# Kernel optimization log

Hardware: AMD Instinct MI355X
Metric: run time of the kernel (lower is better)

Reference implementation:

```python
import jax, jax.numpy as jnp
import numpy as np

B, H, S, D = 2, 16, 2048, 64


def setup_inputs() -> dict:
    key = jax.random.key(0)
    kq, kk, kv = jax.random.split(key, 3)
    q = jax.random.normal(kq, (B, H, S, D), dtype=jnp.float32)
    k = jax.random.normal(kk, (B, H, S, D), dtype=jnp.float32)
    v = jax.random.normal(kv, (B, H, S, D), dtype=jnp.float32)
    # look-ahead (causal) mask: 1 where attention is NOT allowed (future positions)
    mask = 1.0 - jnp.tril(jnp.ones((S, S), dtype=jnp.float32))
    mask = mask[None, None, :, :]  # broadcastable to (B, H, S, S)
    return {"q": q, "k": k, "v": v, "mask": mask}


def reference(q, k, v, mask):
    # scores: (B, H, Sq, Sk)
    dk = jnp.asarray(q.shape[-1], dtype=q.dtype)
    logits = jnp.einsum("bhqd,bhkd->bhqk", q, k) / jnp.sqrt(dk)
    logits = logits + mask * (-1e9)
    attn = jax.nn.softmax(logits, axis=-1)
    # dropout rate 0.0 / inference mode -> identity
    out = jnp.einsum("bhqk,bhkd->bhqd", attn, v)
    return out, attn
```

## Files before the change

### kernel.cpp

```cpp
#include <hip/hip_runtime.h>


typedef __attribute__((ext_vector_type(4))) float f32x4;
typedef __attribute__((ext_vector_type(8))) short bf16x8;

#define S_LEN 2048
#define D_DIM 64
#define LDK   72
#define SCALE 0.125f

__device__ __forceinline__ unsigned int f2bf1(float f) {
  unsigned int u = __float_as_uint(f);
  return (u + 0x7FFFu + ((u >> 16) & 1u)) >> 16;
}
__device__ __forceinline__ unsigned long long pack4bf(float a, float b, float c, float d) {
  unsigned int lo = f2bf1(a) | (f2bf1(b) << 16);
  unsigned int hi = f2bf1(c) | (f2bf1(d) << 16);
  return (unsigned long long)lo | ((unsigned long long)hi << 32);
}

__global__ __launch_bounds__(256, 4)
void attn_fused(const float* __restrict__ Qg, const float* __restrict__ Kg,
                const float* __restrict__ Vg, float* __restrict__ Og,
                float* __restrict__ Ag)
{
  __shared__ __attribute__((aligned(16))) unsigned short qs[64 * LDK];
  __shared__ __attribute__((aligned(16))) unsigned short ks[64 * LDK];
  __shared__ __attribute__((aligned(16))) unsigned short vs[64 * LDK];
  __shared__ __attribute__((aligned(16))) unsigned short ps[4 * 16 * LDK];

  const int tid  = threadIdx.x;
  const int lane = tid & 63;
  const int w    = tid >> 6;
  const int l15  = lane & 15;
  const int lg   = lane >> 4;
  const int bh   = blockIdx.x & 31;
  const int q0   = (blockIdx.x >> 5) << 6;

  const float* qb = Qg + (size_t)bh * S_LEN * D_DIM;
  const float* kb = Kg + (size_t)bh * S_LEN * D_DIM;
  const float* vb = Vg + (size_t)bh * S_LEN * D_DIM;
  float* ob = Og + (size_t)bh * S_LEN * D_DIM;
  float* ab = Ag + (size_t)bh * S_LEN * S_LEN;

#pragma unroll
  for (int j = 0; j < 4; ++j) {
    int f = tid + j * 256;
    int row = f >> 4, dg = f & 15;
    float4 v = *(const float4*)(qb + (q0 + row) * D_DIM + dg * 4);
    *(unsigned long long*)(qs + row * LDK + dg * 4) = pack4bf(v.x, v.y, v.z, v.w);
  }
  __syncthreads();
  const bf16x8 qf0 = *(const bf16x8*)(qs + (w * 16 + l15) * LDK + lg * 8);
  const bf16x8 qf1 = *(const bf16x8*)(qs + (w * 16 + l15) * LDK + 32 + lg * 8);

  const int ktiles = (q0 >> 6) + 1;
  const int qr0 = q0 + w * 16 + lg * 4;

  float lsum[4] = {0.f, 0.f, 0.f, 0.f};
  for (int t = 0; t < ktiles; ++t) {
    const int kt = t << 6;
    __syncthreads();
#pragma unroll
    for (int j = 0; j < 4; ++j) {
      int f = tid + j * 256;
      int row = f >> 4, dg = f & 15;
      float4 v = *(const float4*)(kb + (kt + row) * D_DIM + dg * 4);
      *(unsigned long long*)(ks + row * LDK + dg * 4) = pack4bf(v.x, v.y, v.z, v.w);
    }
    __syncthreads();
#pragma unroll
    for (int kbk = 0; kbk < 4; ++kbk) {
      const bf16x8 kf0 = *(const bf16x8*)(ks + (kbk * 16 + l15) * LDK + lg * 8);
      const bf16x8 kf1 = *(const bf16x8*)(ks + (kbk * 16 + l15) * LDK + 32 + lg * 8);
      f32x4 s = {0.f, 0.f, 0.f, 0.f};
      s = __builtin_amdgcn_mfma_f32_16x16x32_bf16(qf0, kf0, s, 0, 0, 0);
      s = __builtin_amdgcn_mfma_f32_16x16x32_bf16(qf1, kf1, s, 0, 0, 0);
      const int kc = kt + kbk * 16 + l15;
#pragma unroll
      for (int r = 0; r < 4; ++r)
        lsum[r] += (kc <= qr0 + r) ? __expf(s[r] * SCALE) : 0.f;
    }
  }
#pragma unroll
  for (int m = 1; m < 16; m <<= 1) {
#pragma unroll
    for (int r = 0; r < 4; ++r) lsum[r] += __shfl_xor(lsum[r], m, 64);
  }
  float ri[4];
#pragma unroll
  for (int r = 0; r < 4; ++r) ri[r] = 1.f / lsum[r];

  f32x4 o[4];
#pragma unroll
  for (int d = 0; d < 4; ++d) o[d] = (f32x4){0.f, 0.f, 0.f, 0.f};

  unsigned short* pw = ps + w * 16 * LDK;

  for (int t = 0; t < ktiles; ++t) {
    const int kt = t << 6;
    __syncthreads();
#pragma unroll
    for (int j = 0; j < 4; ++j) {
      int f = tid + j * 256;
      int row = f >> 4, dg = f & 15;
      float4 v = *(const float4*)(kb + (kt + row) * D_DIM + dg * 4);
      *(unsigned long long*)(ks + row * LDK + dg * 4) = pack4bf(v.x, v.y, v.z, v.w);
    }
    {
      const int kb4 = tid >> 4, db4 = tid & 15;
      const float* vsrc = vb + (kt + kb4 * 4) * D_DIM + db4 * 4;
      float4 r0 = *(const float4*)(vsrc);
      float4 r1 = *(const float4*)(vsrc + D_DIM);
      float4 r2 = *(const float4*)(vsrc + 2 * D_DIM);
      float4 r3 = *(const float4*)(vsrc + 3 * D_DIM);
      *(unsigned long long*)(vs + (db4 * 4 + 0) * LDK + kb4 * 4) = pack4bf(r0.x, r1.x, r2.x, r3.x);
      *(unsigned long long*)(vs + (db4 * 4 + 1) * LDK + kb4 * 4) = pack4bf(r0.y, r1.y, r2.y, r3.y);
      *(unsigned long long*)(vs + (db4 * 4 + 2) * LDK + kb4 * 4) = pack4bf(r0.z, r1.z, r2.z, r3.z);
      *(unsigned long long*)(vs + (db4 * 4 + 3) * LDK + kb4 * 4) = pack4bf(r0.w, r1.w, r2.w, r3.w);
    }
    __syncthreads();

#pragma unroll
    for (int kbk = 0; kbk < 4; ++kbk) {
      const bf16x8 kf0 = *(const bf16x8*)(ks + (kbk * 16 + l15) * LDK + lg * 8);
      const bf16x8 kf1 = *(const bf16x8*)(ks + (kbk * 16 + l15) * LDK + 32 + lg * 8);
      f32x4 s = {0.f, 0.f, 0.f, 0.f};
      s = __builtin_amdgcn_mfma_f32_16x16x32_bf16(qf0, kf0, s, 0, 0, 0);
      s = __builtin_amdgcn_mfma_f32_16x16x32_bf16(qf1, kf1, s, 0, 0, 0);
      const int kc = kt + kbk * 16 + l15;
#pragma unroll
      for (int r = 0; r < 4; ++r) {
        float p = (kc <= qr0 + r) ? __expf(s[r] * SCALE) * ri[r] : 0.f;
        pw[(lg * 4 + r) * LDK + kbk * 16 + l15] = (unsigned short)f2bf1(p);
      }
    }
    asm volatile("s_waitcnt lgkmcnt(0)" ::: "memory");

#pragma unroll
    for (int j = 0; j < 4; ++j) {
      const int row = j * 4 + lg;
      uint2 pk2 = *(const uint2*)(pw + row * LDK + l15 * 4);
      f32x4 fv;
      fv.x = __uint_as_float((pk2.x & 0xFFFFu) << 16);
      fv.y = __uint_as_float(pk2.x & 0xFFFF0000u);
      fv.z = __uint_as_float((pk2.y & 0xFFFFu) << 16);
      fv.w = __uint_as_float(pk2.y & 0xFFFF0000u);
      __builtin_nontemporal_store(fv,
        (f32x4*)(ab + (size_t)(q0 + w * 16 + row) * S_LEN + kt + l15 * 4));
    }

    const bf16x8 pa0 = *(const bf16x8*)(pw + l15 * LDK + lg * 8);
    const bf16x8 pa1 = *(const bf16x8*)(pw + l15 * LDK + 32 + lg * 8);
#pragma unroll
    for (int d = 0; d < 4; ++d) {
      const bf16x8 vf0 = *(const bf16x8*)(vs + (d * 16 + l15) * LDK + lg * 8);
      const bf16x8 vf1 = *(const bf16x8*)(vs + (d * 16 + l15) * LDK + 32 + lg * 8);
      o[d] = __builtin_amdgcn_mfma_f32_16x16x32_bf16(pa0, vf0, o[d], 0, 0, 0);
      o[d] = __builtin_amdgcn_mfma_f32_16x16x32_bf16(pa1, vf1, o[d], 0, 0, 0);
    }
  }

  {
    const f32x4 z = (f32x4){0.f, 0.f, 0.f, 0.f};
#pragma unroll
    for (int j = 0; j < 4; ++j) {
      const int qrow = q0 + w * 16 + j * 4 + lg;
      float* rp = ab + (size_t)qrow * S_LEN;
      for (int c = q0 + 64 + l15 * 4; c < S_LEN; c += 64)
        __builtin_nontemporal_store(z, (f32x4*)(rp + c));
    }
  }

#pragma unroll
  for (int r = 0; r < 4; ++r) {
    float* rp = ob + (size_t)(qr0 + r) * D_DIM + l15;
    rp[0]  = o[0][r];
    rp[16] = o[1][r];
    rp[32] = o[2][r];
    rp[48] = o[3][r];
  }
}

extern "C" void kernel_launch(void* const* d_in, const int* in_sizes, int n_in,
                              void* d_out, int out_size, void* d_ws, size_t ws_size,
                              hipStream_t stream) {
  (void)in_sizes; (void)n_in; (void)d_ws; (void)ws_size; (void)out_size;
  const float* q = (const float*)d_in[0];
  const float* k = (const float*)d_in[1];
  const float* v = (const float*)d_in[2];
  float* out  = (float*)d_out;
  float* attn = out + (size_t)2 * 16 * 2048 * 64;
  attn_fused<<<dim3(32 * 32), dim3(256), 0, stream>>>(q, k, v, out, attn);
}
```

Before: 160.5 us.

## Pair causal query tiles per block and double-buffer K/V loads

Each block now handles two query tiles, jq and 31-jq, so every block does the same total causal work, and the grid is halved to 512 blocks. K and V tiles are double-buffered in shared memory: the next tile's global loads are issued before the current tile's MFMA work and written to the alternate buffer afterwards, which removes one barrier per iteration. Launch bounds drop to 2 blocks per SM, allowing more registers for the prefetch registers but lowering occupancy. The per-tile attention output stores and zero fills are unchanged.

```diff
diff --git a/kernel.cpp b/kernel.cpp
--- a/kernel.cpp
+++ b/kernel.cpp
@@ -19,23 +19,22 @@
   return (unsigned long long)lo | ((unsigned long long)hi << 32);
 }
 
-__global__ __launch_bounds__(256, 4)
+__global__ __launch_bounds__(256, 2)
 void attn_fused(const float* __restrict__ Qg, const float* __restrict__ Kg,
                 const float* __restrict__ Vg, float* __restrict__ Og,
                 float* __restrict__ Ag)
 {
   __shared__ __attribute__((aligned(16))) unsigned short qs[64 * LDK];
-  __shared__ __attribute__((aligned(16))) unsigned short ks[64 * LDK];
-  __shared__ __attribute__((aligned(16))) unsigned short vs[64 * LDK];
+  __shared__ __attribute__((aligned(16))) unsigned short ks[2][64 * LDK];
+  __shared__ __attribute__((aligned(16))) unsigned short vs[2][64 * LDK];
   __shared__ __attribute__((aligned(16))) unsigned short ps[4 * 16 * LDK];
 
   const int tid  = threadIdx.x;
-  const int lane = tid & 63;
   const int w    = tid >> 6;
-  const int l15  = lane & 15;
-  const int lg   = lane >> 4;
+  const int l15  = tid & 15;
+  const int lg   = (tid >> 4) & 3;
   const int bh   = blockIdx.x & 31;
-  const int q0   = (blockIdx.x >> 5) << 6;
+  const int pj   = blockIdx.x >> 5;
 
   const float* qb = Qg + (size_t)bh * S_LEN * D_DIM;
   const float* kb = Kg + (size_t)bh * S_LEN * D_DIM;
@@ -43,142 +42,202 @@
   float* ob = Og + (size_t)bh * S_LEN * D_DIM;
   float* ab = Ag + (size_t)bh * S_LEN * S_LEN;
 
-#pragma unroll
-  for (int j = 0; j < 4; ++j) {
-    int f = tid + j * 256;
-    int row = f >> 4, dg = f & 15;
-    float4 v = *(const float4*)(qb + (q0 + row) * D_DIM + dg * 4);
-    *(unsigned long long*)(qs + row * LDK + dg * 4) = pack4bf(v.x, v.y, v.z, v.w);
-  }
-  __syncthreads();
-  const bf16x8 qf0 = *(const bf16x8*)(qs + (w * 16 + l15) * LDK + lg * 8);
-  const bf16x8 qf1 = *(const bf16x8*)(qs + (w * 16 + l15) * LDK + 32 + lg * 8);
-
-  const int ktiles = (q0 >> 6) + 1;
-  const int qr0 = q0 + w * 16 + lg * 4;
-
-  float lsum[4] = {0.f, 0.f, 0.f, 0.f};
-  for (int t = 0; t < ktiles; ++t) {
-    const int kt = t << 6;
-    __syncthreads();
-#pragma unroll
-    for (int j = 0; j < 4; ++j) {
-      int f = tid + j * 256;
+  unsigned short* pw = ps + w * 16 * LDK;
+
+  for (int sel = 0; sel < 2; ++sel) {
+    const int jq  = sel ? (31 - pj) : pj;
+    const int q0  = jq << 6;
+    const int T   = jq + 1;
+    const int qr0 = q0 + w * 16 + lg * 4;
+
+    __syncthreads();
+#pragma unroll
+    for (int jj = 0; jj < 4; ++jj) {
+      int f = tid + jj * 256;
       int row = f >> 4, dg = f & 15;
-      float4 v = *(const float4*)(kb + (kt + row) * D_DIM + dg * 4);
-      *(unsigned long long*)(ks + row * LDK + dg * 4) = pack4bf(v.x, v.y, v.z, v.w);
-    }
-    __syncthreads();
-#pragma unroll
-    for (int kbk = 0; kbk < 4; ++kbk) {
-      const bf16x8 kf0 = *(const bf16x8*)(ks + (kbk * 16 + l15) * LDK + lg * 8);
-      const bf16x8 kf1 = *(const bf16x8*)(ks + (kbk * 16 + l15) * LDK + 32 + lg * 8);
-      f32x4 s = {0.f, 0.f, 0.f, 0.f};
-      s = __builtin_amdgcn_mfma_f32_16x16x32_bf16(qf0, kf0, s, 0, 0, 0);
-      s = __builtin_amdgcn_mfma_f32_16x16x32_bf16(qf1, kf1, s, 0, 0, 0);
-      const int kc = kt + kbk * 16 + l15;
-#pragma unroll
-      for (int r = 0; r < 4; ++r)
-        lsum[r] += (kc <= qr0 + r) ? __expf(s[r] * SCALE) : 0.f;
-    }
-  }
-#pragma unroll
-  for (int m = 1; m < 16; m <<= 1) {
-#pragma unroll
-    for (int r = 0; r < 4; ++r) lsum[r] += __shfl_xor(lsum[r], m, 64);
-  }
-  float ri[4];
-#pragma unroll
-  for (int r = 0; r < 4; ++r) ri[r] = 1.f / lsum[r];
-
-  f32x4 o[4];
-#pragma unroll
-  for (int d = 0; d < 4; ++d) o[d] = (f32x4){0.f, 0.f, 0.f, 0.f};
-
-  unsigned short* pw = ps + w * 16 * LDK;
-
-  for (int t = 0; t < ktiles; ++t) {
-    const int kt = t << 6;
-    __syncthreads();
-#pragma unroll
-    for (int j = 0; j < 4; ++j) {
-      int f = tid + j * 256;
+      float4 v = *(const float4*)(qb + (q0 + row) * D_DIM + dg * 4);
+      *(unsigned long long*)(qs + row * LDK + dg * 4) = pack4bf(v.x, v.y, v.z, v.w);
+    }
+    __syncthreads();
+    const bf16x8 qf0 = *(const bf16x8*)(qs + (w * 16 + l15) * LDK + lg * 8);
+    const bf16x8 qf1 = *(const bf16x8*)(qs + (w * 16 + l15) * LDK + 32 + lg * 8);
+
+    float lsum[4] = {0.f, 0.f, 0.f, 0.f};
+#pragma unroll
+    for (int jj = 0; jj < 4; ++jj) {
+      int f = tid + jj * 256;
       int row = f >> 4, dg = f & 15;
-      float4 v = *(const float4*)(kb + (kt + row) * D_DIM + dg * 4);
-      *(unsigned long long*)(ks + row * LDK + dg * 4) = pack4bf(v.x, v.y, v.z, v.w);
+      float4 v = *(const float4*)(kb + row * D_DIM + dg * 4);
+      *(unsigned long long*)(ks[0] + row * LDK + dg * 4) = pack4bf(v.x, v.y, v.z, v.w);
+    }
+    __syncthreads();
+    int cur = 0;
+    for (int t = 0; t < T; ++t) {
+      const int kt = t << 6;
+      const bool pf = (t + 1 < T);
+      float4 kl[4];
+      if (pf) {
+#pragma unroll
+        for (int jj = 0; jj < 4; ++jj) {
+          int f = tid + jj * 256;
+          int row = f >> 4, dg = f & 15;
+          kl[jj] = *(const float4*)(kb + (kt + 64 + row) * D_DIM + dg * 4);
+        }
+      }
+      const unsigned short* kcur = ks[cur];
+#pragma unroll
+      for (int kbk = 0; kbk < 4; ++kbk) {
+        const bf16x8 kf0 = *(const bf16x8*)(kcur + (kbk * 16 + l15) * LDK + lg * 8);
+        const bf16x8 kf1 = *(const bf16x8*)(kcur + (kbk * 16 + l15) * LDK + 32 + lg * 8);
+        f32x4 s = {0.f, 0.f, 0.f, 0.f};
+        s = __builtin_amdgcn_mfma_f32_16x16x32_bf16(qf0, kf0, s, 0, 0, 0);
+        s = __builtin_amdgcn_mfma_f32_16x16x32_bf16(qf1, kf1, s, 0, 0, 0);
+        const int kc = kt + kbk * 16 + l15;
+#pragma unroll
+        for (int r = 0; r < 4; ++r)
+          lsum[r] += (kc <= qr0 + r) ? __expf(s[r] * SCALE) : 0.f;
+      }
+      if (pf) {
+#pragma unroll
+        for (int jj = 0; jj < 4; ++jj) {
+          int f = tid + jj * 256;
+          int row = f >> 4, dg = f & 15;
+          *(unsigned long long*)(ks[cur ^ 1] + row * LDK + dg * 4) =
+              pack4bf(kl[jj].x, kl[jj].y, kl[jj].z, kl[jj].w);
+        }
+      }
+      __syncthreads();
+      cur ^= 1;
+    }
+#pragma unroll
+    for (int m = 1; m < 16; m <<= 1) {
+#pragma unroll
+      for (int r = 0; r < 4; ++r) lsum[r] += __shfl_xor(lsum[r], m, 64);
+    }
+    float ri[4];
+#pragma unroll
+    for (int r = 0; r < 4; ++r) ri[r] = 1.f / lsum[r];
+
+    f32x4 o[4];
+#pragma unroll
+    for (int d = 0; d < 4; ++d) o[d] = (f32x4){0.f, 0.f, 0.f, 0.f};
+
+#pragma unroll
+    for (int jj = 0; jj < 4; ++jj) {
+      int f = tid + jj * 256;
+      int row = f >> 4, dg = f & 15;
+      float4 v = *(const float4*)(kb + row * D_DIM + dg * 4);
+      *(unsigned long long*)(ks[0] + row * LDK + dg * 4) = pack4bf(v.x, v.y, v.z, v.w);
     }
     {
       const int kb4 = tid >> 4, db4 = tid & 15;
-      const float* vsrc = vb + (kt + kb4 * 4) * D_DIM + db4 * 4;
+      const float* vsrc = vb + (kb4 * 4) * D_DIM + db4 * 4;
       float4 r0 = *(const float4*)(vsrc);
       float4 r1 = *(const float4*)(vsrc + D_DIM);
       float4 r2 = *(const float4*)(vsrc + 2 * D_DIM);
       float4 r3 = *(const float4*)(vsrc + 3 * D_DIM);
-      *(unsigned long long*)(vs + (db4 * 4 + 0) * LDK + kb4 * 4) = pack4bf(r0.x, r1.x, r2.x, r3.x);
-      *(unsigned long long*)(vs + (db4 * 4 + 1) * LDK + kb4 * 4) = pack4bf(r0.y, r1.y, r2.y, r3.y);
-      *(unsigned long long*)(vs + (db4 * 4 + 2) * LDK + kb4 * 4) = pack4bf(r0.z, r1.z, r2.z, r3.z);
-      *(unsigned long long*)(vs + (db4 * 4 + 3) * LDK + kb4 * 4) = pack4bf(r0.w, r1.w, r2.w, r3.w);
-    }
-    __syncthreads();
-
-#pragma unroll
-    for (int kbk = 0; kbk < 4; ++kbk) {
-      const bf16x8 kf0 = *(const bf16x8*)(ks + (kbk * 16 + l15) * LDK + lg * 8);
-      const bf16x8 kf1 = *(const bf16x8*)(ks + (kbk * 16 + l15) * LDK + 32 + lg * 8);
-      f32x4 s = {0.f, 0.f, 0.f, 0.f};
-      s = __builtin_amdgcn_mfma_f32_16x16x32_bf16(qf0, kf0, s, 0, 0, 0);
-      s = __builtin_amdgcn_mfma_f32_16x16x32_bf16(qf1, kf1, s, 0, 0, 0);
-      const int kc = kt + kbk * 16 + l15;
-#pragma unroll
-      for (int r = 0; r < 4; ++r) {
-        float p = (kc <= qr0 + r) ? __expf(s[r] * SCALE) * ri[r] : 0.f;
-        pw[(lg * 4 + r) * LDK + kbk * 16 + l15] = (unsigned short)f2bf1(p);
-      }
-    }
-    asm volatile("s_waitcnt lgkmcnt(0)" ::: "memory");
-
-#pragma unroll
-    for (int j = 0; j < 4; ++j) {
-      const int row = j * 4 + lg;
-      uint2 pk2 = *(const uint2*)(pw + row * LDK + l15 * 4);
-      f32x4 fv;
-      fv.x = __uint_as_float((pk2.x & 0xFFFFu) << 16);
-      fv.y = __uint_as_float(pk2.x & 0xFFFF0000u);
-      fv.z = __uint_as_float((pk2.y & 0xFFFFu) << 16);
-      fv.w = __uint_as_float(pk2.y & 0xFFFF0000u);
-      __builtin_nontemporal_store(fv,
-        (f32x4*)(ab + (size_t)(q0 + w * 16 + row) * S_LEN + kt + l15 * 4));
-    }
-
-    const bf16x8 pa0 = *(const bf16x8*)(pw + l15 * LDK + lg * 8);
-    const bf16x8 pa1 = *(const bf16x8*)(pw + l15 * LDK + 32 + lg * 8);
-#pragma unroll
-    for (int d = 0; d < 4; ++d) {
-      const bf16x8 vf0 = *(const bf16x8*)(vs + (d * 16 + l15) * LDK + lg * 8);
-      const bf16x8 vf1 = *(const bf16x8*)(vs + (d * 16 + l15) * LDK + 32 + lg * 8);
-      o[d] = __builtin_amdgcn_mfma_f32_16x16x32_bf16(pa0, vf0, o[d], 0, 0, 0);
-      o[d] = __builtin_amdgcn_mfma_f32_16x16x32_bf16(pa1, vf1, o[d], 0, 0, 0);
-    }
-  }
-
-  {
-    const f32x4 z = (f32x4){0.f, 0.f, 0.f, 0.f};
-#pragma unroll
-    for (int j = 0; j < 4; ++j) {
-      const int qrow = q0 + w * 16 + j * 4 + lg;
-      float* rp = ab + (size_t)qrow * S_LEN;
-      for (int c = q0 + 64 + l15 * 4; c < S_LEN; c += 64)
-        __builtin_nontemporal_store(z, (f32x4*)(rp + c));
-    }
-  }
-
-#pragma unroll
-  for (int r = 0; r < 4; ++r) {
-    float* rp = ob + (size_t)(qr0 + r) * D_DIM + l15;
-    rp[0]  = o[0][r];
-    rp[16] = o[1][r];
-    rp[32] = o[2][r];
-    rp[48] = o[3][r];
+      *(unsigned long long*)(vs[0] + (db4 * 4 + 0) * LDK + kb4 * 4) = pack4bf(r0.x, r1.x, r2.x, r3.x);
+      *(unsigned long long*)(vs[0] + (db4 * 4 + 1) * LDK + kb4 * 4) = pack4bf(r0.y, r1.y, r2.y, r3.y);
+      *(unsigned long long*)(vs[0] + (db4 * 4 + 2) * LDK + kb4 * 4) = pack4bf(r0.z, r1.z, r2.z, r3.z);
+      *(unsigned long long*)(vs[0] + (db4 * 4 + 3) * LDK + kb4 * 4) = pack4bf(r0.w, r1.w, r2.w, r3.w);
+    }
+    __syncthreads();
+    cur = 0;
+    for (int t = 0; t < T; ++t) {
+      const int kt = t << 6;
+      const bool pf = (t + 1 < T);
+      float4 kl[4], v0, v1, v2, v3;
+      if (pf) {
+#pragma unroll
+        for (int jj = 0; jj < 4; ++jj) {
+          int f = tid + jj * 256;
+          int row = f >> 4, dg = f & 15;
+          kl[jj] = *(const float4*)(kb + (kt + 64 + row) * D_DIM + dg * 4);
+        }
+        const int kb4 = tid >> 4, db4 = tid & 15;
+        const float* vsrc = vb + (kt + 64 + kb4 * 4) * D_DIM + db4 * 4;
+        v0 = *(const float4*)(vsrc);
+        v1 = *(const float4*)(vsrc + D_DIM);
+        v2 = *(const float4*)(vsrc + 2 * D_DIM);
+        v3 = *(const float4*)(vsrc + 3 * D_DIM);
+      }
+      const unsigned short* kcur = ks[cur];
+#pragma unroll
+      for (int kbk = 0; kbk < 4; ++kbk) {
+        const bf16x8 kf0 = *(const bf16x8*)(kcur + (kbk * 16 + l15) * LDK + lg * 8);
+        const bf16x8 kf1 = *(const bf16x8*)(kcur + (kbk * 16 + l15) * LDK + 32 + lg * 8);
+        f32x4 s = {0.f, 0.f, 0.f, 0.f};
+        s = __builtin_amdgcn_mfma_f32_16x16x32_bf16(qf0, kf0, s, 0, 0, 0);
+        s = __builtin_amdgcn_mfma_f32_16x16x32_bf16(qf1, kf1, s, 0, 0, 0);
+        const int kc = kt + kbk * 16 + l15;
+#pragma unroll
+        for (int r = 0; r < 4; ++r) {
+          float p = (kc <= qr0 + r) ? __expf(s[r] * SCALE) * ri[r] : 0.f;
+          pw[(lg * 4 + r) * LDK + kbk * 16 + l15] = (unsigned short)f2bf1(p);
+        }
+      }
+      asm volatile("s_waitcnt lgkmcnt(0)" ::: "memory");
+
+#pragma unroll
+      for (int jj = 0; jj < 4; ++jj) {
+        const int row = jj * 4 + lg;
+        uint2 pk2 = *(const uint2*)(pw + row * LDK + l15 * 4);
+        f32x4 fv;
+        fv.x = __uint_as_float((pk2.x & 0xFFFFu) << 16);
+        fv.y = __uint_as_float(pk2.x & 0xFFFF0000u);
+        fv.z = __uint_as_float((pk2.y & 0xFFFFu) << 16);
+        fv.w = __uint_as_float(pk2.y & 0xFFFF0000u);
+        __builtin_nontemporal_store(fv,
+          (f32x4*)(ab + (size_t)(q0 + w * 16 + row) * S_LEN + kt + l15 * 4));
+      }
+
+      const bf16x8 pa0 = *(const bf16x8*)(pw + l15 * LDK + lg * 8);
+      const bf16x8 pa1 = *(const bf16x8*)(pw + l15 * LDK + 32 + lg * 8);
+      const unsigned short* vcur = vs[cur];
+#pragma unroll
+      for (int d = 0; d < 4; ++d) {
+        const bf16x8 vf0 = *(const bf16x8*)(vcur + (d * 16 + l15) * LDK + lg * 8);
+        const bf16x8 vf1 = *(const bf16x8*)(vcur + (d * 16 + l15) * LDK + 32 + lg * 8);
+        o[d] = __builtin_amdgcn_mfma_f32_16x16x32_bf16(pa0, vf0, o[d], 0, 0, 0);
+        o[d] = __builtin_amdgcn_mfma_f32_16x16x32_bf16(pa1, vf1, o[d], 0, 0, 0);
+      }
+      if (pf) {
+#pragma unroll
+        for (int jj = 0; jj < 4; ++jj) {
+          int f = tid + jj * 256;
+          int row = f >> 4, dg = f & 15;
+          *(unsigned long long*)(ks[cur ^ 1] + row * LDK + dg * 4) =
+              pack4bf(kl[jj].x, kl[jj].y, kl[jj].z, kl[jj].w);
+        }
+        const int kb4 = tid >> 4, db4 = tid & 15;
+        *(unsigned long long*)(vs[cur ^ 1] + (db4 * 4 + 0) * LDK + kb4 * 4) = pack4bf(v0.x, v1.x, v2.x, v3.x);
+        *(unsigned long long*)(vs[cur ^ 1] + (db4 * 4 + 1) * LDK + kb4 * 4) = pack4bf(v0.y, v1.y, v2.y, v3.y);
+        *(unsigned long long*)(vs[cur ^ 1] + (db4 * 4 + 2) * LDK + kb4 * 4) = pack4bf(v0.z, v1.z, v2.z, v3.z);
+        *(unsigned long long*)(vs[cur ^ 1] + (db4 * 4 + 3) * LDK + kb4 * 4) = pack4bf(v0.w, v1.w, v2.w, v3.w);
+      }
+      __syncthreads();
+      cur ^= 1;
+    }
+
+    {
+      const f32x4 z = (f32x4){0.f, 0.f, 0.f, 0.f};
+#pragma unroll
+      for (int jj = 0; jj < 4; ++jj) {
+        const int qrow = q0 + w * 16 + jj * 4 + lg;
+        float* rp = ab + (size_t)qrow * S_LEN;
+        for (int c = q0 + 64 + l15 * 4; c < S_LEN; c += 64)
+          __builtin_nontemporal_store(z, (f32x4*)(rp + c));
+      }
+    }
+
+#pragma unroll
+    for (int r = 0; r < 4; ++r) {
+      float* rp = ob + (size_t)(qr0 + r) * D_DIM + l15;
+      rp[0]  = o[0][r];
+      rp[16] = o[1][r];
+      rp[32] = o[2][r];
+      rp[48] = o[3][r];
+    }
   }
 }
 
@@ -191,5 +250,5 @@
   const float* v = (const float*)d_in[2];
   float* out  = (float*)d_out;
   float* attn = out + (size_t)2 * 16 * 2048 * 64;
-  attn_fused<<<dim3(32 * 32), dim3(256), 0, stream>>>(q, k, v, out, attn);
-}
+  attn_fused<<<dim3(512), dim3(256), 0, stream>>>(q, k, v, out, attn);
+}
```

Result: faster. 144.3 us (-10.1%).
